# Optimization experiments

Measured on AMD Instinct MI355X. Metric: run time of the kernel, lower is better.

Reference implementation:

```python
import jax, jax.numpy as jnp
import numpy as np

DIM = 256
NUM_HEADS = 8
HEAD_DIM = DIM // NUM_HEADS


def setup_inputs() -> dict:
    key = jax.random.key(0)
    k1, k2, k3, k4 = jax.random.split(key, 4)
    B, C, H, W = 16, DIM, 64, 64
    x = jax.random.normal(k1, (B, C, H, W), dtype=jnp.float32)
    # 1x1 convs as dense weight matrices [out_ch, in_ch]
    Wqkv = jax.random.normal(k2, (3 * DIM, DIM), dtype=jnp.float32) * (DIM ** -0.5)
    Wproj = jax.random.normal(k3, (DIM, DIM), dtype=jnp.float32) * (DIM ** -0.5)
    bproj = jax.random.normal(k4, (DIM,), dtype=jnp.float32) * 0.01
    return {"x": x, "Wqkv": Wqkv, "Wproj": Wproj, "bproj": bproj}


def reference(x, Wqkv, Wproj, bproj):
    B, C, H, W = x.shape
    N = H * W
    hd = C // NUM_HEADS

    # qkv: 1x1 conv (no bias) == channel matmul
    qkv = jnp.einsum('oc,bchw->bohw', Wqkv, x)  # [B, 3C, H, W]
    q, k, v = jnp.split(qkv, 3, axis=1)

    def to_heads(t):
        # b (h d) x y -> b h (x y) d
        return t.reshape(B, NUM_HEADS, hd, N).transpose(0, 1, 3, 2)

    q, k, v = to_heads(q), to_heads(k), to_heads(v)  # [B, h, N, d]

    # linear attention feature map + per-token normalization over d
    q = jax.nn.elu(q) + 1.0
    k = jax.nn.elu(k) + 1.0
    q = q / jnp.sum(q, axis=-1, keepdims=True)
    k = k / jnp.sum(k, axis=-1, keepdims=True)

    kv = jnp.einsum('bhnd,bhne->bhde', k, v)   # [B, h, d, d]
    out = jnp.einsum('bhnd,bhde->bhne', q, kv)  # [B, h, N, d]

    # b h (x y) d -> b (h d) x y
    out = out.transpose(0, 1, 3, 2).reshape(B, C, H, W)

    # proj: 1x1 conv with bias; drop_path is identity in eval mode
    out = jnp.einsum('oc,bchw->bohw', Wproj, out) + bproj[None, :, None, None]
    return out + x
```

## Files before the change

kernel.cpp:

```cpp
#include <hip/hip_runtime.h>
#include <stdint.h>
#include <stddef.h>

#define DIM   256
#define NH    8
#define HD    32
#define BATCH 16
#define NTOK  4096

typedef __attribute__((ext_vector_type(8))) short short8;
typedef __attribute__((ext_vector_type(4))) float f32x4;

__device__ __forceinline__ unsigned short f2bf(float x){
  unsigned u = __float_as_uint(x);
  u += 0x7fffu + ((u >> 16) & 1u);
  return (unsigned short)(u >> 16);
}
__device__ __forceinline__ float elu1(float v){
  return (v > 0.f) ? (v + 1.f) : __expf(v);
}
__device__ __forceinline__ void gload_lds16(const void* g, void* lds){
  __builtin_amdgcn_global_load_lds(
      (const __attribute__((address_space(1))) unsigned int*)g,
      (__attribute__((address_space(3))) unsigned int*)lds, 16, 0, 0);
}

__global__ __launch_bounds__(256) void k_transpose_x(const float* __restrict__ x,
                                                     unsigned short* __restrict__ xt){
  __shared__ float tile[64][65];
  const int b = blockIdx.z, c0 = blockIdx.y * 64, n0 = blockIdx.x * 64;
  const float* xb = x + (size_t)b * DIM * NTOK;
  const int t = threadIdx.x;
  #pragma unroll
  for (int p = 0; p < 4; p++){
    int idx = t + p * 256;
    int row = idx >> 4;
    int col = (idx & 15) << 2;
    float4 v = *(const float4*)(xb + (size_t)(c0 + row) * NTOK + n0 + col);
    tile[row][col] = v.x; tile[row][col+1] = v.y; tile[row][col+2] = v.z; tile[row][col+3] = v.w;
  }
  __syncthreads();
  unsigned short* xtb = xt + (size_t)b * NTOK * DIM;
  #pragma unroll
  for (int p = 0; p < 4; p++){
    int idx = t + p * 256;
    int nl = idx >> 4;
    int cl = (idx & 15) << 2;
    ushort4 o;
    o.x = f2bf(tile[cl+0][nl]); o.y = f2bf(tile[cl+1][nl]);
    o.z = f2bf(tile[cl+2][nl]); o.w = f2bf(tile[cl+3][nl]);
    *(ushort4*)(xtb + (size_t)(n0 + nl) * DIM + c0 + cl) = o;
  }
}

__global__ __launch_bounds__(256) void k_convert_w(const float* __restrict__ wqkv,
                                                   unsigned short* __restrict__ wq_bf){
  int i = blockIdx.x * 256 + threadIdx.x;
  int row = i >> 6;
  int c4 = (i & 63) * 4;
  int dst;
  if (row < 256)      dst = row;
  else if (row < 512){ int p = (row - 256) >> 6; int s = (row - 256) & 63; dst = 256 + p*128 + s; }
  else               { int p = (row - 512) >> 6; int s = (row - 512) & 63; dst = 256 + p*128 + 64 + s; }
  float4 v = *(const float4*)(wqkv + (size_t)row * DIM + c4);
  ushort4 o = { f2bf(v.x), f2bf(v.y), f2bf(v.z), f2bf(v.w) };
  *(ushort4*)(wq_bf + (size_t)dst * DIM + c4) = o;
}

__global__ __launch_bounds__(512, 1) void k_qkv10(const unsigned short* __restrict__ wbf,
                                                  const unsigned short* __restrict__ xt,
                                                  unsigned short* __restrict__ qn,
                                                  float* __restrict__ kvp){
  __shared__ __align__(16) unsigned short sh[33792];
  unsigned short* bsh = sh + 16384;
  const int t = threadIdx.x;
  const int w = t >> 6, l = t & 63;
  const int t16 = l & 15, quad = l >> 4;
  const int wm = w >> 1, wn = w & 1;
  const int bid = blockIdx.x;
  const int super = bid / 48;
  const int rem = bid - super * 48;
  const int m = rem >> 3, lx = rem & 7;
  const int chunk = super * 8 + lx;
  const int b = chunk >> 4, nt2 = chunk & 15;
  const int o0 = m * 128;
  const bool isQ = (o0 < 256);
  const unsigned short* Bb = xt + ((size_t)b * NTOK + (size_t)nt2 * 256) * DIM;
  const int rowL = (w*16 + t16) * DIM + quad*8;

  short8 a_reg[4][2][2];
  {
    const unsigned short* srcA = wbf + (size_t)(o0 + w*16 + t16) * DIM + quad*8;
    #pragma unroll
    for (int c = 0; c < 4; c++){
      gload_lds16(srcA + c*64,      sh + (w*8 + c*2 + 0)*512);
      gload_lds16(srcA + c*64 + 32, sh + (w*8 + c*2 + 1)*512);
    }
    asm volatile("s_waitcnt vmcnt(0)" ::: "memory");
    __builtin_amdgcn_s_barrier();
    #pragma unroll
    for (int c = 0; c < 4; c++)
      #pragma unroll
      for (int i = 0; i < 2; i++)
        #pragma unroll
        for (int kk = 0; kk < 2; kk++)
          a_reg[c][i][kk] = *(const short8*)(sh + ((wm*2 + i)*8 + c*2 + kk)*512 + l*8);
    asm volatile("s_waitcnt lgkmcnt(0)" ::: "memory");
    __builtin_amdgcn_s_barrier();
  }

#define STAGE(ss) { \
    const unsigned short* srcB = Bb + (size_t)(((ss) >> 2)*128) * DIM + rowL + ((ss) & 3)*64; \
    unsigned short* db = sh + ((ss) & 1) * 8192; \
    gload_lds16(srcB,      db + (w*2 + 0)*512); \
    gload_lds16(srcB + 32, db + (w*2 + 1)*512); }

  STAGE(0); STAGE(1);

  f32x4 acc[2][4];
  #pragma unroll
  for (int i = 0; i < 2; i++)
    #pragma unroll
    for (int j = 0; j < 4; j++){ acc[i][j][0]=0.f; acc[i][j][1]=0.f; acc[i][j][2]=0.f; acc[i][j][3]=0.f; }
  f32x4 kvacc;
  kvacc[0]=0.f; kvacc[1]=0.f; kvacc[2]=0.f; kvacc[3]=0.f;

  #pragma unroll
  for (int s = 0; s < 8; s++){
    if (s < 4)       { asm volatile("s_waitcnt vmcnt(2)" ::: "memory"); }
    else if (s < 6)  { if (isQ) { asm volatile("s_waitcnt vmcnt(6)" ::: "memory"); }
                       else     { asm volatile("s_waitcnt vmcnt(2)" ::: "memory"); } }
    else if (s == 6) { asm volatile("s_waitcnt vmcnt(2)" ::: "memory"); }
    else             { asm volatile("s_waitcnt vmcnt(0)" ::: "memory"); }
    __builtin_amdgcn_s_barrier();
    const unsigned short* bufc = sh + (s & 1) * 8192;
    #pragma unroll
    for (int kk = 0; kk < 2; kk++){
      short8 bb[4];
      #pragma unroll
      for (int j = 0; j < 4; j++) bb[j] = *(const short8*)(bufc + ((wn*4 + j)*2 + kk)*512 + l*8);
      #pragma unroll
      for (int i = 0; i < 2; i++)
        #pragma unroll
        for (int j = 0; j < 4; j++)
          acc[i][j] = __builtin_amdgcn_mfma_f32_16x16x32_bf16(a_reg[s&3][i][kk], bb[j], acc[i][j], 0, 0, 0);
    }
    __builtin_amdgcn_s_barrier();
    if (s < 6) STAGE(s + 2);

    if ((s & 3) == 3){
      const int n0 = (nt2*2 + (s >> 2)) * 128;
      if (isQ || wm < 2){
        #pragma unroll
        for (int i = 0; i < 2; i++)
          #pragma unroll
          for (int j = 0; j < 4; j++)
            #pragma unroll
            for (int r = 0; r < 4; r++) acc[i][j][r] = elu1(acc[i][j][r]);
        float sc[4];
        #pragma unroll
        for (int j = 0; j < 4; j++){
          float v = 0.f;
          #pragma unroll
          for (int i = 0; i < 2; i++)
            #pragma unroll
            for (int r = 0; r < 4; r++) v += acc[i][j][r];
          v += __shfl_xor(v, 16);
          v += __shfl_xor(v, 32);
          sc[j] = 1.0f / v;
        }
        #pragma unroll
        for (int i = 0; i < 2; i++)
          #pragma unroll
          for (int j = 0; j < 4; j++){
            float inv = sc[j];
            #pragma unroll
            for (int r = 0; r < 4; r++) acc[i][j][r] *= inv;
          }
      }
      if (isQ){
        #pragma unroll
        for (int i = 0; i < 2; i++)
          #pragma unroll
          for (int j = 0; j < 4; j++){
            int n_l = wn*64 + j*16 + t16;
            int o_l0 = wm*32 + i*16 + quad*4;
            ushort4 pk = { f2bf(acc[i][j][0]), f2bf(acc[i][j][1]),
                           f2bf(acc[i][j][2]), f2bf(acc[i][j][3]) };
            *(ushort4*)(bsh + n_l*136 + o_l0) = pk;
          }
        asm volatile("s_waitcnt lgkmcnt(0)" ::: "memory");
        __builtin_amdgcn_s_barrier();
        unsigned short* dst = qn + (size_t)b * NTOK * DIM;
        #pragma unroll
        for (int p2 = 0; p2 < 4; p2++){
          int gg = t + p2 * 512;
          int n_l = gg >> 4, c = gg & 15;
          uint4 v = *(const uint4*)(bsh + n_l*136 + c*8);
          *(uint4*)(dst + (size_t)(n0 + n_l) * DIM + o0 + c*8) = v;
        }
      } else {
        #pragma unroll
        for (int i = 0; i < 2; i++)
          #pragma unroll
          for (int j = 0; j < 4; j++){
            int n_l = wn*64 + j*16 + t16;
            #pragma unroll
            for (int r = 0; r < 4; r++){
              int o_l = wm*32 + i*16 + quad*4 + r;
              bsh[o_l*136 + n_l] = f2bf(acc[i][j][r]);
            }
          }
        asm volatile("s_waitcnt lgkmcnt(0)" ::: "memory");
        __builtin_amdgcn_s_barrier();
        const int hl = w >> 2, dh = (w >> 1) & 1, eh = w & 1;
        const unsigned short* kbase = bsh + (hl*32 + dh*16) * 136;
        const unsigned short* vbase = bsh + (64 + hl*32 + eh*16) * 136;
        #pragma unroll
        for (int kk2 = 0; kk2 < 4; kk2++){
          int nn = kk2*32 + quad*8;
          short8 afrag = *(const short8*)(kbase + t16*136 + nn);
          short8 bfrag = *(const short8*)(vbase + t16*136 + nn);
          kvacc = __builtin_amdgcn_mfma_f32_16x16x32_bf16(afrag, bfrag, kvacc, 0, 0, 0);
        }
      }
      if (s == 3){
        #pragma unroll
        for (int i = 0; i < 2; i++)
          #pragma unroll
          for (int j = 0; j < 4; j++){ acc[i][j][0]=0.f; acc[i][j][1]=0.f; acc[i][j][2]=0.f; acc[i][j][3]=0.f; }
      }
    }
  }
#undef STAGE

  if (!isQ){
    const int pp = (o0 >> 7) - 2;
    const int hl = w >> 2, dh = (w >> 1) & 1, eh = w & 1;
    float* dst = kvp + ((size_t)((b*8 + pp*2 + hl) * 16 + nt2)) * 1024;
    #pragma unroll
    for (int r = 0; r < 4; r++)
      dst[(dh*16 + quad*4 + r)*32 + eh*16 + t16] = kvacc[r];
  }
}

__global__ __launch_bounds__(256) void k_M(const float* __restrict__ kvp,
                                           const float* __restrict__ wproj,
                                           unsigned short* __restrict__ M){
  __shared__ float kvL[1024];
  __shared__ float wpL[8192];
  const int t = threadIdx.x;
  const int h = blockIdx.x, b = blockIdx.y;
  const float* pbase = kvp + (size_t)((b*8 + h) * 16) * 1024;
  {
    float4 a = {0.f,0.f,0.f,0.f};
    #pragma unroll
    for (int p = 0; p < 16; p++){
      float4 v = *(const float4*)(pbase + (size_t)p*1024 + t*4);
      a.x += v.x; a.y += v.y; a.z += v.z; a.w += v.w;
    }
    *(float4*)(kvL + t*4) = a;
  }
  #pragma unroll
  for (int p = 0; p < 8; p++){
    int idx = t + p * 256;
    int o = idx >> 3, e4 = idx & 7;
    *(float4*)(wpL + o*32 + e4*4) = *(const float4*)(wproj + (size_t)o * DIM + h*32 + e4*4);
  }
  __syncthreads();
  float wr[32];
  #pragma unroll
  for (int e = 0; e < 32; e++) wr[e] = wpL[t*32 + e];
  unsigned short md[32];
  #pragma unroll
  for (int d = 0; d < 32; d++){
    float a = 0.f;
    #pragma unroll
    for (int e = 0; e < 32; e++) a += wr[e] * kvL[d*32 + e];
    md[d] = f2bf(a);
  }
  unsigned short* dst = M + (size_t)b * 65536 + (size_t)t * DIM + h*32;
  #pragma unroll
  for (int q = 0; q < 4; q++) *(uint4*)(dst + q*8) = *(const uint4*)(md + q*8);
}

__global__ __launch_bounds__(512, 4) void k_out5(const unsigned short* __restrict__ M,
                                                 const unsigned short* __restrict__ qn,
                                                 const float* __restrict__ x,
                                                 const float* __restrict__ bproj,
                                                 float* __restrict__ out){
  __shared__ __align__(16) unsigned short As[8192];
  __shared__ __align__(16) unsigned short Bs[8192];
  const int t = threadIdx.x;
  const int w = t >> 6, l = t & 63;
  const int t16 = l & 15, quad = l >> 4;
  const int wm = w >> 1, wn = w & 1;
  const int bid = blockIdx.x;
  const int super = bid >> 4;
  const int rem = bid & 15;
  const int m = rem >> 3, lx = rem & 7;
  const int g = super * 8 + lx;
  const int nt = g >> 4, b = g & 15;
  const int o0 = m * 128, n0 = nt * 128;
  const unsigned short* A = qn + (size_t)b * NTOK * DIM;
  const unsigned short* Bm = M + (size_t)b * 65536;

  f32x4 acc[2][4];
  #pragma unroll
  for (int i = 0; i < 2; i++)
    #pragma unroll
    for (int j = 0; j < 4; j++){ acc[i][j][0]=0.f; acc[i][j][1]=0.f; acc[i][j][2]=0.f; acc[i][j][3]=0.f; }

  for (int k0 = 0; k0 < 256; k0 += 64){
    __syncthreads();
    #pragma unroll
    for (int s4 = 0; s4 < 4; s4++){
      int s = w * 4 + s4;
      int sl = s & 15;
      int tile = sl >> 1, kk = sl & 1;
      const unsigned short* src = (s < 16)
          ? (A  + (size_t)(n0 + tile*16 + t16) * DIM + k0 + kk*32 + quad*8)
          : (Bm + (size_t)(o0 + tile*16 + t16) * DIM + k0 + kk*32 + quad*8);
      gload_lds16(src, (s < 16) ? (As + sl * 512) : (Bs + sl * 512));
    }
    __syncthreads();
    #pragma unroll
    for (int kk = 0; kk < 2; kk++){
      short8 a[2], bb[4];
      #pragma unroll
      for (int i = 0; i < 2; i++) a[i]  = *(const short8*)(As + ((wm*2 + i)*2 + kk) * 512 + l * 8);
      #pragma unroll
      for (int j = 0; j < 4; j++) bb[j] = *(const short8*)(Bs + ((wn*4 + j)*2 + kk) * 512 + l * 8);
      #pragma unroll
      for (int i = 0; i < 2; i++)
        #pragma unroll
        for (int j = 0; j < 4; j++)
          acc[i][j] = __builtin_amdgcn_mfma_f32_16x16x32_bf16(a[i], bb[j], acc[i][j], 0, 0, 0);
    }
  }

  const float* xb = x + (size_t)b * DIM * NTOK;
  float* ob = out + (size_t)b * DIM * NTOK;
  #pragma unroll
  for (int j = 0; j < 4; j++){
    int o = o0 + wn*64 + j*16 + t16;
    float bias = bproj[o];
    #pragma unroll
    for (int i = 0; i < 2; i++){
      int n = n0 + wm*32 + i*16 + quad*4;
      float4 xv = *(const float4*)(xb + (size_t)o * NTOK + n);
      float4 res = { acc[i][j][0] + bias + xv.x,
                     acc[i][j][1] + bias + xv.y,
                     acc[i][j][2] + bias + xv.z,
                     acc[i][j][3] + bias + xv.w };
      *(float4*)(ob + (size_t)o * NTOK + n) = res;
    }
  }
}

extern "C" void kernel_launch(void* const* d_in, const int* in_sizes, int n_in,
                              void* d_out, int out_size, void* d_ws, size_t ws_size,
                              hipStream_t stream){
  const float* x     = (const float*)d_in[0];
  const float* wqkv  = (const float*)d_in[1];
  const float* wproj = (const float*)d_in[2];
  const float* bproj = (const float*)d_in[3];
  float* out = (float*)d_out;
  char* ws = (char*)d_ws;

  unsigned short* xt   = (unsigned short*)(ws);
  unsigned short* qn   = (unsigned short*)(ws + ((size_t)32 << 20));
  float* kvp           = (float*)(ws + ((size_t)64 << 20));
  unsigned short* M    = (unsigned short*)(ws + ((size_t)80 << 20));
  unsigned short* wqbf = (unsigned short*)(ws + ((size_t)82 << 20));

  k_transpose_x<<<dim3(64, 4, 16), 256, 0, stream>>>(x, xt);
  k_convert_w  <<<dim3(192), 256, 0, stream>>>(wqkv, wqbf);
  k_qkv10      <<<dim3(1536), 512, 0, stream>>>(wqbf, xt, qn, kvp);
  k_M          <<<dim3(8, 16), 256, 0, stream>>>(kvp, wproj, M);
  k_out5       <<<dim3(1024), 512, 0, stream>>>(M, qn, x, bproj, out);
}
```

Measured before the change: 220.3 us.

## Merge prep kernels, raise MFMA priority, and enlarge output GEMM tile

The x transpose and weight conversion are merged into one launch, using an extra grid z-slice for the weight blocks. This removes a kernel launch and its gap. The QKV kernel wraps its MFMA loop in s_setprio(1)/s_setprio(0) so the matrix math is favoured over other waves' memory ops. The output projection kernel doubles its token tile to 256 with a 4x4 accumulator per wave and halves the grid, so each loaded M tile is reused more, at the cost of more registers and LDS and occupancy lowered to 2.

```diff
diff --git a/kernel.cpp b/kernel.cpp
--- a/kernel.cpp
+++ b/kernel.cpp
@@ -25,49 +25,52 @@
       (__attribute__((address_space(3))) unsigned int*)lds, 16, 0, 0);
 }
 
-__global__ __launch_bounds__(256) void k_transpose_x(const float* __restrict__ x,
-                                                     unsigned short* __restrict__ xt){
-  __shared__ float tile[64][65];
-  const int b = blockIdx.z, c0 = blockIdx.y * 64, n0 = blockIdx.x * 64;
-  const float* xb = x + (size_t)b * DIM * NTOK;
+__global__ __launch_bounds__(256) void k_prep(const float* __restrict__ x,
+                                              unsigned short* __restrict__ xt,
+                                              const float* __restrict__ wqkv,
+                                              unsigned short* __restrict__ wq_bf){
   const int t = threadIdx.x;
-  #pragma unroll
-  for (int p = 0; p < 4; p++){
-    int idx = t + p * 256;
-    int row = idx >> 4;
-    int col = (idx & 15) << 2;
-    float4 v = *(const float4*)(xb + (size_t)(c0 + row) * NTOK + n0 + col);
-    tile[row][col] = v.x; tile[row][col+1] = v.y; tile[row][col+2] = v.z; tile[row][col+3] = v.w;
-  }
-  __syncthreads();
-  unsigned short* xtb = xt + (size_t)b * NTOK * DIM;
-  #pragma unroll
-  for (int p = 0; p < 4; p++){
-    int idx = t + p * 256;
-    int nl = idx >> 4;
-    int cl = (idx & 15) << 2;
-    ushort4 o;
-    o.x = f2bf(tile[cl+0][nl]); o.y = f2bf(tile[cl+1][nl]);
-    o.z = f2bf(tile[cl+2][nl]); o.w = f2bf(tile[cl+3][nl]);
-    *(ushort4*)(xtb + (size_t)(n0 + nl) * DIM + c0 + cl) = o;
-  }
-}
-
-__global__ __launch_bounds__(256) void k_convert_w(const float* __restrict__ wqkv,
-                                                   unsigned short* __restrict__ wq_bf){
-  int i = blockIdx.x * 256 + threadIdx.x;
-  int row = i >> 6;
-  int c4 = (i & 63) * 4;
-  int dst;
-  if (row < 256)      dst = row;
-  else if (row < 512){ int p = (row - 256) >> 6; int s = (row - 256) & 63; dst = 256 + p*128 + s; }
-  else               { int p = (row - 512) >> 6; int s = (row - 512) & 63; dst = 256 + p*128 + 64 + s; }
-  float4 v = *(const float4*)(wqkv + (size_t)row * DIM + c4);
-  ushort4 o = { f2bf(v.x), f2bf(v.y), f2bf(v.z), f2bf(v.w) };
-  *(ushort4*)(wq_bf + (size_t)dst * DIM + c4) = o;
-}
-
-__global__ __launch_bounds__(512, 1) void k_qkv10(const unsigned short* __restrict__ wbf,
+  if (blockIdx.z < 16){
+    __shared__ float tile[64][65];
+    const int b = blockIdx.z, c0 = blockIdx.y * 64, n0 = blockIdx.x * 64;
+    const float* xb = x + (size_t)b * DIM * NTOK;
+    #pragma unroll
+    for (int p = 0; p < 4; p++){
+      int idx = t + p * 256;
+      int row = idx >> 4;
+      int col = (idx & 15) << 2;
+      float4 v = *(const float4*)(xb + (size_t)(c0 + row) * NTOK + n0 + col);
+      tile[row][col] = v.x; tile[row][col+1] = v.y; tile[row][col+2] = v.z; tile[row][col+3] = v.w;
+    }
+    __syncthreads();
+    unsigned short* xtb = xt + (size_t)b * NTOK * DIM;
+    #pragma unroll
+    for (int p = 0; p < 4; p++){
+      int idx = t + p * 256;
+      int nl = idx >> 4;
+      int cl = (idx & 15) << 2;
+      ushort4 o;
+      o.x = f2bf(tile[cl+0][nl]); o.y = f2bf(tile[cl+1][nl]);
+      o.z = f2bf(tile[cl+2][nl]); o.w = f2bf(tile[cl+3][nl]);
+      *(ushort4*)(xtb + (size_t)(n0 + nl) * DIM + c0 + cl) = o;
+    }
+  } else {
+    const int blk = blockIdx.y * 64 + blockIdx.x;
+    if (blk >= 192) return;
+    int i = blk * 256 + t;
+    int row = i >> 6;
+    int c4 = (i & 63) * 4;
+    int dst;
+    if (row < 256)      dst = row;
+    else if (row < 512){ int p = (row - 256) >> 6; int s = (row - 256) & 63; dst = 256 + p*128 + s; }
+    else               { int p = (row - 512) >> 6; int s = (row - 512) & 63; dst = 256 + p*128 + 64 + s; }
+    float4 v = *(const float4*)(wqkv + (size_t)row * DIM + c4);
+    ushort4 o = { f2bf(v.x), f2bf(v.y), f2bf(v.z), f2bf(v.w) };
+    *(ushort4*)(wq_bf + (size_t)dst * DIM + c4) = o;
+  }
+}
+
+__global__ __launch_bounds__(512, 1) void k_qkv11(const unsigned short* __restrict__ wbf,
                                                   const unsigned short* __restrict__ xt,
                                                   unsigned short* __restrict__ qn,
                                                   float* __restrict__ kvp){
@@ -134,6 +137,7 @@
     else             { asm volatile("s_waitcnt vmcnt(0)" ::: "memory"); }
     __builtin_amdgcn_s_barrier();
     const unsigned short* bufc = sh + (s & 1) * 8192;
+    __builtin_amdgcn_s_setprio(1);
     #pragma unroll
     for (int kk = 0; kk < 2; kk++){
       short8 bb[4];
@@ -145,6 +149,7 @@
         for (int j = 0; j < 4; j++)
           acc[i][j] = __builtin_amdgcn_mfma_f32_16x16x32_bf16(a_reg[s&3][i][kk], bb[j], acc[i][j], 0, 0, 0);
     }
+    __builtin_amdgcn_s_setprio(0);
     __builtin_amdgcn_s_barrier();
     if (s < 6) STAGE(s + 2);
 
@@ -284,12 +289,12 @@
   for (int q = 0; q < 4; q++) *(uint4*)(dst + q*8) = *(const uint4*)(md + q*8);
 }
 
-__global__ __launch_bounds__(512, 4) void k_out5(const unsigned short* __restrict__ M,
+__global__ __launch_bounds__(512, 2) void k_out6(const unsigned short* __restrict__ M,
                                                  const unsigned short* __restrict__ qn,
                                                  const float* __restrict__ x,
                                                  const float* __restrict__ bproj,
                                                  float* __restrict__ out){
-  __shared__ __align__(16) unsigned short As[8192];
+  __shared__ __align__(16) unsigned short As[16384];
   __shared__ __align__(16) unsigned short Bs[8192];
   const int t = threadIdx.x;
   const int w = t >> 6, l = t & 63;
@@ -301,13 +306,13 @@
   const int m = rem >> 3, lx = rem & 7;
   const int g = super * 8 + lx;
   const int nt = g >> 4, b = g & 15;
-  const int o0 = m * 128, n0 = nt * 128;
+  const int o0 = m * 128, n0 = nt * 256;
   const unsigned short* A = qn + (size_t)b * NTOK * DIM;
   const unsigned short* Bm = M + (size_t)b * 65536;
 
-  f32x4 acc[2][4];
-  #pragma unroll
-  for (int i = 0; i < 2; i++)
+  f32x4 acc[4][4];
+  #pragma unroll
+  for (int i = 0; i < 4; i++)
     #pragma unroll
     for (int j = 0; j < 4; j++){ acc[i][j][0]=0.f; acc[i][j][1]=0.f; acc[i][j][2]=0.f; acc[i][j][3]=0.f; }
 
@@ -315,24 +320,26 @@
     __syncthreads();
     #pragma unroll
     for (int s4 = 0; s4 < 4; s4++){
-      int s = w * 4 + s4;
-      int sl = s & 15;
+      int sl = w*4 + s4;
       int tile = sl >> 1, kk = sl & 1;
-      const unsigned short* src = (s < 16)
-          ? (A  + (size_t)(n0 + tile*16 + t16) * DIM + k0 + kk*32 + quad*8)
-          : (Bm + (size_t)(o0 + tile*16 + t16) * DIM + k0 + kk*32 + quad*8);
-      gload_lds16(src, (s < 16) ? (As + sl * 512) : (Bs + sl * 512));
+      gload_lds16(A + (size_t)(n0 + tile*16 + t16) * DIM + k0 + kk*32 + quad*8, As + sl*512);
+    }
+    #pragma unroll
+    for (int s2 = 0; s2 < 2; s2++){
+      int sl = w*2 + s2;
+      int tile = sl >> 1, kk = sl & 1;
+      gload_lds16(Bm + (size_t)(o0 + tile*16 + t16) * DIM + k0 + kk*32 + quad*8, Bs + sl*512);
     }
     __syncthreads();
     #pragma unroll
     for (int kk = 0; kk < 2; kk++){
-      short8 a[2], bb[4];
-      #pragma unroll
-      for (int i = 0; i < 2; i++) a[i]  = *(const short8*)(As + ((wm*2 + i)*2 + kk) * 512 + l * 8);
+      short8 a[4], bb[4];
+      #pragma unroll
+      for (int i = 0; i < 4; i++) a[i]  = *(const short8*)(As + ((wm*4 + i)*2 + kk) * 512 + l * 8);
       #pragma unroll
       for (int j = 0; j < 4; j++) bb[j] = *(const short8*)(Bs + ((wn*4 + j)*2 + kk) * 512 + l * 8);
       #pragma unroll
-      for (int i = 0; i < 2; i++)
+      for (int i = 0; i < 4; i++)
         #pragma unroll
         for (int j = 0; j < 4; j++)
           acc[i][j] = __builtin_amdgcn_mfma_f32_16x16x32_bf16(a[i], bb[j], acc[i][j], 0, 0, 0);
@@ -346,8 +353,8 @@
     int o = o0 + wn*64 + j*16 + t16;
     float bias = bproj[o];
     #pragma unroll
-    for (int i = 0; i < 2; i++){
-      int n = n0 + wm*32 + i*16 + quad*4;
+    for (int i = 0; i < 4; i++){
+      int n = n0 + wm*64 + i*16 + quad*4;
       float4 xv = *(const float4*)(xb + (size_t)o * NTOK + n);
       float4 res = { acc[i][j][0] + bias + xv.x,
                      acc[i][j][1] + bias + xv.y,
@@ -374,9 +381,8 @@
   unsigned short* M    = (unsigned short*)(ws + ((size_t)80 << 20));
   unsigned short* wqbf = (unsigned short*)(ws + ((size_t)82 << 20));
 
-  k_transpose_x<<<dim3(64, 4, 16), 256, 0, stream>>>(x, xt);
-  k_convert_w  <<<dim3(192), 256, 0, stream>>>(wqkv, wqbf);
-  k_qkv10      <<<dim3(1536), 512, 0, stream>>>(wqbf, xt, qn, kvp);
-  k_M          <<<dim3(8, 16), 256, 0, stream>>>(kvp, wproj, M);
-  k_out5       <<<dim3(1024), 512, 0, stream>>>(M, qn, x, bproj, out);
-}
+  k_prep  <<<dim3(64, 4, 17), 256, 0, stream>>>(x, xt, wqkv, wqbf);
+  k_qkv11 <<<dim3(1536), 512, 0, stream>>>(wqbf, xt, qn, kvp);
+  k_M     <<<dim3(8, 16), 256, 0, stream>>>(kvp, wproj, M);
+  k_out6  <<<dim3(512), 512, 0, stream>>>(M, qn, x, bproj, out);
+}
```

Result: no change. 219.9 us (-0.2%).
